# Kernel tuning notes

Hardware: AMD Instinct MI355X
Metric: run time of the kernel (lower is better)

The kernel has to match this reference:

```python
import jax, jax.numpy as jnp
import numpy as np

N = 50000   # num_entities
E = 600000  # num_edges
D = 128     # dim
R = 200     # num_relations
T = 1000    # num_timestamps
L = 2       # num_layers


def setup_inputs() -> dict:
    key = jax.random.key(0)
    ks = jax.random.split(key, 16)
    edge_index = jax.random.randint(ks[0], (2, E), 0, N)
    edge_type = jax.random.randint(ks[1], (E,), 0, R)
    edge_time = jax.random.randint(ks[2], (E,), 0, T)
    edge_weight = jax.random.uniform(ks[3], (E,), dtype=jnp.float32)
    perm = jax.random.permutation(ks[4], N)
    entity_emb = jax.random.normal(ks[5], (N, D), dtype=jnp.float32)
    rel_emb = jax.random.normal(ks[6], (R, D), dtype=jnp.float32)
    time_emb = jax.random.normal(ks[7], (T, D), dtype=jnp.float32)
    s = 1.0 / np.sqrt(D)
    in_proj_w = jax.random.uniform(ks[8], (L, D, 2 * D), minval=-s, maxval=s)
    in_proj_b = jax.random.uniform(ks[9], (L, 2 * D), minval=-s, maxval=s)
    out_proj_w = jax.random.uniform(ks[10], (L, D, D), minval=-s, maxval=s)
    out_proj_b = jax.random.uniform(ks[11], (L, D), minval=-s, maxval=s)
    A = jax.random.normal(ks[12], (L, D)) * 0.1
    B = jax.random.normal(ks[13], (L, D)) * 0.1
    ln_g = jnp.ones((L, D), dtype=jnp.float32)
    ln_b = jnp.zeros((L, D), dtype=jnp.float32)
    return dict(edge_index=edge_index, edge_type=edge_type, edge_time=edge_time,
                edge_weight=edge_weight, perm=perm, entity_emb=entity_emb,
                rel_emb=rel_emb, time_emb=time_emb, in_proj_w=in_proj_w,
                in_proj_b=in_proj_b, out_proj_w=out_proj_w, out_proj_b=out_proj_b,
                A=A, B=B, ln_g=ln_g, ln_b=ln_b)


def _mamba_layer(x, Wi, bi, Wo, bo, A, B, g_ln, b_ln):
    # x: [N, D]
    zg = x @ Wi + bi                      # [N, 2D]
    z, g = jnp.split(zg, 2, axis=-1)
    g = jax.nn.sigmoid(g)

    def step(prev, zg_i):
        z_i, g_i = zg_i
        curr = g_i * (A * prev) + B * z_i
        return curr, curr

    _, h = jax.lax.scan(step, jnp.zeros((D,), x.dtype), (z, g))  # [N, D]
    y = x + h @ Wo + bo
    mu = jnp.mean(y, axis=-1, keepdims=True)
    var = jnp.mean((y - mu) ** 2, axis=-1, keepdims=True)
    return (y - mu) / jnp.sqrt(var + 1e-5) * g_ln + b_ln


def reference(edge_index, edge_type, edge_time, edge_weight, perm, entity_emb,
              rel_emb, time_emb, in_proj_w, in_proj_b, out_proj_w, out_proj_b,
              A, B, ln_g, ln_b):
    src, dst = edge_index[0], edge_index[1]
    msgs = entity_emb[src] + rel_emb[edge_type] + time_emb[edge_time]  # [E, D]
    sums = jax.ops.segment_sum(msgs * edge_weight[:, None], dst, num_segments=N)
    cnt = jax.ops.segment_sum(edge_weight, dst, num_segments=N)
    x = sums / jnp.maximum(cnt, 1.0)[:, None]          # scatter_mean
    x = x / jnp.maximum(jnp.linalg.norm(x, axis=1, keepdims=True), 1e-12)
    x = x[perm]
    for l in range(L):
        x = _mamba_layer(x, in_proj_w[l], in_proj_b[l], out_proj_w[l],
                         out_proj_b[l], A[l], B[l], ln_g[l], ln_b[l])
    return x
```

## Files before the change

### kernel.cpp

```cpp
#include <hip/hip_runtime.h>
#include <hip/hip_bf16.h>

typedef unsigned short ushort_t;
typedef unsigned int   uint_t;
typedef __attribute__((ext_vector_type(8))) short bf8;
typedef __attribute__((ext_vector_type(4))) float f32x4;

constexpr int N = 50000;
constexpr int E = 600000;
constexpr int D = 128;
constexpr int L = 2;
constexpr int NB = (N + 255) / 256;

constexpr int RB   = 80;
constexpr int RBLK = N / RB;
constexpr int LOOK = 16;
constexpr int CSTR = 136;
constexpr int CROWS = RB + LOOK;

__device__ __forceinline__ float us2f(ushort_t u) {
    union { uint_t i; float f; } c; c.i = (uint_t)u << 16; return c.f;
}
__device__ __forceinline__ float u2f(uint_t u) {
    union { uint_t i; float f; } c; c.i = u; return c.f;
}
__device__ __forceinline__ ushort_t f2us(float f) {
    __hip_bfloat16 b = __float2bfloat16(f);
    return *(ushort_t*)&b;
}

__global__ __launch_bounds__(256) void k_alloc(
    const int* __restrict__ hist, int* __restrict__ gcnt,
    int* __restrict__ cursor, int* __restrict__ rowst)
{
    int i = blockIdx.x * 256 + threadIdx.x;
    int v = (i < N) ? hist[i] : 0;
    int lane = threadIdx.x & 63;
    int s = v;
    #pragma unroll
    for (int m = 1; m < 64; m <<= 1) {
        int t = __shfl_up(s, m, 64);
        if (lane >= m) s += t;
    }
    int base = 0;
    if (lane == 63) base = atomicAdd(gcnt, s);
    base = __shfl(base, 63, 64);
    int b = base + s - v;
    if (i < N) {
        cursor[i] = b;
        rowst[i]  = b;
    }
}

__global__ __launch_bounds__(256) void k_scatter(
    const int* __restrict__ eidx, const int* __restrict__ etype,
    const int* __restrict__ etime, const float* __restrict__ ew,
    int* __restrict__ cursor, int2* __restrict__ esort)
{
    int e = blockIdx.x * 256 + threadIdx.x;
    if (e >= E) return;
    int dst = eidx[E + e];
    int slot = atomicAdd(&cursor[dst], 1);
    int2 p;
    p.x = (eidx[e] & 0xffff) | (etype[e] << 16);
    p.y = (etime[e] & 0xffff) | ((int)f2us(ew[e]) << 16);
    esort[slot] = p;
}

constexpr size_t CAST_TBL = 3276800;
constexpr size_t CAST_W   = CAST_TBL + (size_t)L * 256 * 128
                                     + (size_t)L * 128 * 128;
constexpr size_t CAST_H   = CAST_W + E;
constexpr size_t CAST_TOT = CAST_H + N;

__global__ __launch_bounds__(256) void k_cast(
    const float* __restrict__ ent, const float* __restrict__ rel,
    const float* __restrict__ tim, const float* __restrict__ Wi,
    const float* __restrict__ Wo, const int* __restrict__ dstp,
    const int* __restrict__ perm,
    ushort_t* __restrict__ entb, ushort_t* __restrict__ relb,
    ushort_t* __restrict__ timb, ushort_t* __restrict__ WiT,
    ushort_t* __restrict__ WoT, int* __restrict__ hist,
    int* __restrict__ invp)
{
    size_t t = (size_t)blockIdx.x * 256 + threadIdx.x;
    if (t < CAST_TBL) {
        const float2* s; uint_t* d; size_t off;
        if (t < 3200000)      { s = (const float2*)ent; d = (uint_t*)entb; off = t; }
        else if (t < 3212800) { s = (const float2*)rel; d = (uint_t*)relb; off = t - 3200000; }
        else                  { s = (const float2*)tim; d = (uint_t*)timb; off = t - 3212800; }
        float2 v = s[off];
        d[off] = (uint_t)f2us(v.x) | ((uint_t)f2us(v.y) << 16);
    } else if (t < CAST_W) {
        size_t u = t - CAST_TBL;
        if (u < (size_t)L * 256 * 128) {
            int l = u / (256 * 128), r = u % (256 * 128);
            int n = r / 128, k = r % 128;
            WiT[u] = f2us(Wi[(size_t)l * 128 * 256 + k * 256 + n]);
        } else {
            size_t v = u - (size_t)L * 256 * 128;
            int l = v / (128 * 128), r = v % (128 * 128);
            int n = r / 128, k = r % 128;
            WoT[v] = f2us(Wo[(size_t)l * 128 * 128 + k * 128 + n]);
        }
    } else if (t < CAST_H) {
        int e = (int)(t - CAST_W);
        atomicAdd(&hist[dstp[e]], 1);
    } else if (t < CAST_TOT) {
        int i = (int)(t - CAST_H);
        invp[perm[i]] = i;
    }
}

__global__ __launch_bounds__(256) void k_agg(
    const int2* __restrict__ esort, const int* __restrict__ rowst,
    const int* __restrict__ hist, const int* __restrict__ invp,
    const ushort_t* __restrict__ entb, const ushort_t* __restrict__ relb,
    const ushort_t* __restrict__ timb, ushort_t* __restrict__ xbf)
{
    int wv = threadIdx.x >> 6, lane = threadIdx.x & 63;
    int d = blockIdx.x * 4 + wv;
    if (d >= N) return;
    int beg = __builtin_amdgcn_readfirstlane(rowst[d]);
    int n   = __builtin_amdgcn_readfirstlane(hist[d]);

    const uint_t* entu = (const uint_t*)entb;
    const uint_t* relu = (const uint_t*)relb;
    const uint_t* timu = (const uint_t*)timb;

    float s0[4] = {0.f, 0.f, 0.f, 0.f};
    float s1[4] = {0.f, 0.f, 0.f, 0.f};
    float wacc = 0.f;

    for (int c0 = 0; c0 < n; c0 += 64) {
        int mm = n - c0; if (mm > 64) mm = 64;
        int2 rec = esort[beg + c0 + lane];
        uint_t recx = (uint_t)rec.x, recy = (uint_t)rec.y;
        wacc += (lane < mm) ? u2f(recy & 0xffff0000u) : 0.f;

        int j = 0;
        for (; j + 3 < mm; j += 4) {
            #pragma unroll
            for (int u = 0; u < 4; u++) {
                uint_t rx = (uint_t)__builtin_amdgcn_readlane((int)recx, j + u);
                uint_t ry = (uint_t)__builtin_amdgcn_readlane((int)recy, j + u);
                const uint_t* pe = entu + ((size_t)(rx & 0xffffu) << 6);
                const uint_t* pr = relu + ((size_t)(rx >> 16) << 6);
                const uint_t* pt = timu + ((size_t)(ry & 0xffffu) << 6);
                float w = u2f(ry & 0xffff0000u);
                uint_t va = pe[lane];
                uint_t vb = pr[lane];
                uint_t vc = pt[lane];
                float lo = (u2f(va << 16) + u2f(vb << 16)) + u2f(vc << 16);
                float hi = (u2f(va & 0xffff0000u) + u2f(vb & 0xffff0000u))
                         + u2f(vc & 0xffff0000u);
                s0[u] = fmaf(lo, w, s0[u]);
                s1[u] = fmaf(hi, w, s1[u]);
            }
        }
        for (; j < mm; j++) {
            uint_t rx = (uint_t)__builtin_amdgcn_readlane((int)recx, j);
            uint_t ry = (uint_t)__builtin_amdgcn_readlane((int)recy, j);
            const uint_t* pe = entu + ((size_t)(rx & 0xffffu) << 6);
            const uint_t* pr = relu + ((size_t)(rx >> 16) << 6);
            const uint_t* pt = timu + ((size_t)(ry & 0xffffu) << 6);
            float w = u2f(ry & 0xffff0000u);
            uint_t va = pe[lane];
            uint_t vb = pr[lane];
            uint_t vc = pt[lane];
            float lo = (u2f(va << 16) + u2f(vb << 16)) + u2f(vc << 16);
            float hi = (u2f(va & 0xffff0000u) + u2f(vb & 0xffff0000u))
                     + u2f(vc & 0xffff0000u);
            s0[0] = fmaf(lo, w, s0[0]);
            s1[0] = fmaf(hi, w, s1[0]);
        }
    }
    float a0 = (s0[0] + s0[1]) + (s0[2] + s0[3]);
    float a1 = (s1[0] + s1[1]) + (s1[2] + s1[3]);

    float wsum = wacc;
    #pragma unroll
    for (int m = 32; m >= 1; m >>= 1) wsum += __shfl_xor(wsum, m, 64);

    float inv = 1.0f / fmaxf(wsum, 1.0f);
    a0 *= inv; a1 *= inv;

    float ss = a0 * a0 + a1 * a1;
    #pragma unroll
    for (int m = 32; m >= 1; m >>= 1) ss += __shfl_xor(ss, m, 64);
    float sc = 1.0f / fmaxf(sqrtf(ss), 1e-12f);

    int orow = invp[d];
    uint_t out = (uint_t)f2us(a0 * sc) | ((uint_t)f2us(a1 * sc) << 16);
    *(uint_t*)(xbf + (size_t)orow * D + 2 * lane) = out;
}

template <bool FINAL>
__global__ __launch_bounds__(256, 3) void k_layer(
    const ushort_t* __restrict__ xin, const ushort_t* __restrict__ WiT,
    const float* __restrict__ bi, const ushort_t* __restrict__ WoT,
    const float* __restrict__ bo, const float* __restrict__ Aw,
    const float* __restrict__ Bw, const float* __restrict__ lg,
    const float* __restrict__ lb, ushort_t* __restrict__ xoutb,
    float* __restrict__ outf)
{
    __shared__ ushort_t SCA[CROWS * CSTR];
    __shared__ ushort_t SCB[CROWS * CSTR];
    __shared__ float redS[16 * 4], redQ[16 * 4], muA[16], rsA[16];

    int tid = threadIdx.x;
    int w = tid >> 6, lane = tid & 63;
    int quad = lane >> 4, m = lane & 15;
    int r0 = blockIdx.x * RB;

    int cz0 = w * 32 + m, cz1 = cz0 + 16;

    float Ad0 = Aw[cz0], Bd0 = Bw[cz0];
    float Ad1 = Aw[cz1], Bd1 = Bw[cz1];
    float bz0 = bi[cz0], bz1 = bi[cz1];
    float bg0 = bi[cz0 + 128], bg1 = bi[cz1 + 128];

    const f32x4 zero4 = {0.f, 0.f, 0.f, 0.f};

    bf8 Bz0[4], Bz1[4], Bg0[4], Bg1[4];
    #pragma unroll
    for (int kb = 0; kb < 4; kb++) {
        int ko = kb * 32 + quad * 8;
        Bz0[kb] = *(const bf8*)(WiT + (size_t)cz0 * 128 + ko);
        Bz1[kb] = *(const bf8*)(WiT + (size_t)cz1 * 128 + ko);
        Bg0[kb] = *(const bf8*)(WiT + (size_t)(cz0 + 128) * 128 + ko);
        Bg1[kb] = *(const bf8*)(WiT + (size_t)(cz1 + 128) * 128 + ko);
    }

    #pragma unroll
    for (int rt = 0; rt < CROWS / 16; rt++) {
        int gr = r0 - LOOK + rt * 16 + m;
        int grc = gr < 0 ? 0 : gr;
        bf8 a[4];
        #pragma unroll
        for (int kb = 0; kb < 4; kb++)
            a[kb] = *(const bf8*)(xin + (size_t)grc * 128 + kb * 32 + quad * 8);
        f32x4 az0 = zero4, az1 = zero4, ag0 = zero4, ag1 = zero4;
        #pragma unroll
        for (int kb = 0; kb < 4; kb++) {
            az0 = __builtin_amdgcn_mfma_f32_16x16x32_bf16(a[kb], Bz0[kb], az0, 0, 0, 0);
            az1 = __builtin_amdgcn_mfma_f32_16x16x32_bf16(a[kb], Bz1[kb], az1, 0, 0, 0);
            ag0 = __builtin_amdgcn_mfma_f32_16x16x32_bf16(a[kb], Bg0[kb], ag0, 0, 0, 0);
            ag1 = __builtin_amdgcn_mfma_f32_16x16x32_bf16(a[kb], Bg1[kb], ag1, 0, 0, 0);
        }
        #pragma unroll
        for (int reg = 0; reg < 4; reg++) {
            int lr = rt * 16 + quad * 4 + reg;
            float z0 = az0[reg] + bz0, z1 = az1[reg] + bz1;
            float g0 = 1.f / (1.f + __expf(-(ag0[reg] + bg0)));
            float g1 = 1.f / (1.f + __expf(-(ag1[reg] + bg1)));
            SCA[lr * CSTR + cz0] = f2us(g0 * Ad0);
            SCB[lr * CSTR + cz0] = f2us(Bd0 * z0);
            SCA[lr * CSTR + cz1] = f2us(g1 * Ad1);
            SCB[lr * CSTR + cz1] = f2us(Bd1 * z1);
        }
    }
    __syncthreads();

    int dmm = tid & 127;
    float lca[LOOK], lcb[LOOK];
    if (tid >= 128) {
        #pragma unroll
        for (int i = 0; i < LOOK; i++) {
            lca[i] = us2f(SCA[(40 + i) * CSTR + dmm]);
            lcb[i] = us2f(SCB[(40 + i) * CSTR + dmm]);
        }
    }
    __syncthreads();

    if (tid < 128) {
        float h = 0.f;
        #pragma unroll
        for (int i = 0; i < LOOK; i++) {
            int row = r0 - LOOK + i;
            float ca = us2f(SCA[i * CSTR + tid]);
            float cb = us2f(SCB[i * CSTR + tid]);
            h = (row >= 0) ? fmaf(ca, h, cb) : 0.f;
        }
        #pragma unroll 8
        for (int i = LOOK; i < LOOK + 40; i++) {
            float ca = us2f(SCA[i * CSTR + tid]);
            float cb = us2f(SCB[i * CSTR + tid]);
            h = fmaf(ca, h, cb);
            SCA[i * CSTR + tid] = f2us(h);
        }
    } else {
        float h = 0.f;
        #pragma unroll
        for (int i = 0; i < LOOK; i++)
            h = fmaf(lca[i], h, lcb[i]);
        #pragma unroll 8
        for (int i = 56; i < 96; i++) {
            float ca = us2f(SCA[i * CSTR + dmm]);
            float cb = us2f(SCB[i * CSTR + dmm]);
            h = fmaf(ca, h, cb);
            SCA[i * CSTR + dmm] = f2us(h);
        }
    }
    __syncthreads();

    bf8 b0[4], b1[4];
    #pragma unroll
    for (int kb = 0; kb < 4; kb++) {
        int ko = kb * 32 + quad * 8;
        b0[kb] = *(const bf8*)(WoT + (size_t)cz0 * 128 + ko);
        b1[kb] = *(const bf8*)(WoT + (size_t)cz1 * 128 + ko);
    }
    float bias0 = bo[cz0], bias1 = bo[cz1];
    float gl0 = lg[cz0], gl1 = lg[cz1], bl0 = lb[cz0], bl1 = lb[cz1];

    for (int rt = 0; rt < RB / 16; rt++) {
        bf8 a[4];
        #pragma unroll
        for (int kb = 0; kb < 4; kb++)
            a[kb] = *(const bf8*)(SCA + (LOOK + rt * 16 + m) * CSTR
                                      + kb * 32 + quad * 8);
        f32x4 acc0 = {0.f, 0.f, 0.f, 0.f}, acc1 = acc0;
        #pragma unroll
        for (int kb = 0; kb < 4; kb++) {
            acc0 = __builtin_amdgcn_mfma_f32_16x16x32_bf16(a[kb], b0[kb], acc0, 0, 0, 0);
            acc1 = __builtin_amdgcn_mfma_f32_16x16x32_bf16(a[kb], b1[kb], acc1, 0, 0, 0);
        }
        float y0[4], y1[4];
        #pragma unroll
        for (int reg = 0; reg < 4; reg++) {
            int gr = r0 + rt * 16 + quad * 4 + reg;
            y0[reg] = acc0[reg] + bias0 + us2f(xin[(size_t)gr * 128 + cz0]);
            y1[reg] = acc1[reg] + bias1 + us2f(xin[(size_t)gr * 128 + cz1]);
        }
        #pragma unroll
        for (int reg = 0; reg < 4; reg++) {
            float v0 = y0[reg], v1 = y1[reg];
            float s = v0 + v1, q = v0 * v0 + v1 * v1;
            #pragma unroll
            for (int mk = 1; mk <= 8; mk <<= 1) {
                s += __shfl_xor(s, mk, 64);
                q += __shfl_xor(q, mk, 64);
            }
            if (m == 0) {
                int row = quad * 4 + reg;
                redS[row * 4 + w] = s;
                redQ[row * 4 + w] = q;
            }
        }
        __syncthreads();
        if (tid < 16) {
            float s = redS[tid * 4] + redS[tid * 4 + 1] + redS[tid * 4 + 2] + redS[tid * 4 + 3];
            float q = redQ[tid * 4] + redQ[tid * 4 + 1] + redQ[tid * 4 + 2] + redQ[tid * 4 + 3];
            float mu = s * (1.f / 128.f);
            float var = q * (1.f / 128.f) - mu * mu;
            muA[tid] = mu;
            rsA[tid] = rsqrtf(var + 1e-5f);
        }
        __syncthreads();
        #pragma unroll
        for (int reg = 0; reg < 4; reg++) {
            int rr = quad * 4 + reg;
            int gr = r0 + rt * 16 + rr;
            float mu = muA[rr], rs = rsA[rr];
            float v0 = (y0[reg] - mu) * rs * gl0 + bl0;
            float v1 = (y1[reg] - mu) * rs * gl1 + bl1;
            if (FINAL) {
                outf[(size_t)gr * 128 + cz0] = v0;
                outf[(size_t)gr * 128 + cz1] = v1;
            } else {
                xoutb[(size_t)gr * 128 + cz0] = f2us(v0);
                xoutb[(size_t)gr * 128 + cz1] = f2us(v1);
            }
        }
    }
}

extern "C" void kernel_launch(void* const* d_in, const int* in_sizes, int n_in,
                              void* d_out, int out_size, void* d_ws, size_t ws_size,
                              hipStream_t stream)
{
    const int*   eidx  = (const int*)d_in[0];
    const int*   etype = (const int*)d_in[1];
    const int*   etime = (const int*)d_in[2];
    const float* ew    = (const float*)d_in[3];
    const int*   perm  = (const int*)d_in[4];
    const float* ent   = (const float*)d_in[5];
    const float* rel   = (const float*)d_in[6];
    const float* tim   = (const float*)d_in[7];
    const float* Wi    = (const float*)d_in[8];
    const float* bi    = (const float*)d_in[9];
    const float* Wo    = (const float*)d_in[10];
    const float* bo    = (const float*)d_in[11];
    const float* Aw    = (const float*)d_in[12];
    const float* Bw    = (const float*)d_in[13];
    const float* lg    = (const float*)d_in[14];
    const float* lbp   = (const float*)d_in[15];

    char* base = (char*)d_ws;
    size_t o = 0;
    ushort_t* xbf  = (ushort_t*)(base + o); o += (size_t)N * D * 2;
    ushort_t* xb2  = (ushort_t*)(base + o); o += (size_t)N * D * 2;
    ushort_t* entb = (ushort_t*)(base + o); o += (size_t)N * D * 2;
    ushort_t* relb = (ushort_t*)(base + o); o += (size_t)200 * D * 2;
    ushort_t* timb = (ushort_t*)(base + o); o += (size_t)1000 * D * 2;
    ushort_t* WiT  = (ushort_t*)(base + o); o += (size_t)L * 256 * 128 * 2;
    ushort_t* WoT  = (ushort_t*)(base + o); o += (size_t)L * 128 * 128 * 2;
    int2*     esort  = (int2*)(base + o);   o += (size_t)E * 8;
    int*      hist   = (int*)(base + o);    o += (size_t)N * 4;
    int*      gcnt   = (int*)(base + o);    o += 4;
    int*      cursor = (int*)(base + o);    o += (size_t)N * 4;
    int*      rowst  = (int*)(base + o);    o += (size_t)N * 4;
    int*      invp   = (int*)(base + o);    o += (size_t)N * 4;

    hipMemsetAsync(hist, 0, (N + 1) * sizeof(int), stream);

    k_cast    <<<(int)((CAST_TOT + 255) / 256), 256, 0, stream>>>(
                  ent, rel, tim, Wi, Wo, eidx + E, perm,
                  entb, relb, timb, WiT, WoT, hist, invp);
    k_alloc   <<<NB, 256, 0, stream>>>(hist, gcnt, cursor, rowst);
    k_scatter <<<(E + 255) / 256, 256, 0, stream>>>(eidx, etype, etime, ew,
                                                    cursor, esort);
    k_agg     <<<(N + 3) / 4, 256, 0, stream>>>(esort, rowst, hist, invp,
                                                entb, relb, timb, xbf);

    k_layer<false><<<RBLK, 256, 0, stream>>>(
        xbf, WiT, bi, WoT, bo, Aw, Bw, lg, lbp, xb2, nullptr);
    k_layer<true><<<RBLK, 256, 0, stream>>>(
        xb2, WiT + (size_t)256 * 128, bi + 256, WoT + (size_t)128 * 128,
        bo + 128, Aw + 128, Bw + 128, lg + 128, lbp + 128,
        nullptr, (float*)d_out);
}
```

Measured before the change: 283.5 us.

## Fuse preprocessing and layer kernels into persistent kernels with grid barriers

Merges the cast, histogram prefix-alloc, scatter and aggregation kernels into one persistent kernel of 512 blocks separated by software grid barriers. The two layer kernels become one persistent kernel of 416 blocks that loops over row tiles and places a grid barrier between the layers. The aim is to cut kernel launch gaps and tail effects. In exchange it adds barrier spin overhead, reduces occupancy control, and relies on every block being co-resident for the barriers to avoid deadlock.

Result: slower. 845.1 us (+198.1%).

```diff
diff --git a/kernel.cpp b/kernel.cpp
--- a/kernel.cpp
+++ b/kernel.cpp
@@ -10,7 +10,6 @@
 constexpr int E = 600000;
 constexpr int D = 128;
 constexpr int L = 2;
-constexpr int NB = (N + 255) / 256;
 
 constexpr int RB   = 80;
 constexpr int RBLK = N / RB;
@@ -18,54 +17,10 @@
 constexpr int CSTR = 136;
 constexpr int CROWS = RB + LOOK;
 
-__device__ __forceinline__ float us2f(ushort_t u) {
-    union { uint_t i; float f; } c; c.i = (uint_t)u << 16; return c.f;
-}
-__device__ __forceinline__ float u2f(uint_t u) {
-    union { uint_t i; float f; } c; c.i = u; return c.f;
-}
-__device__ __forceinline__ ushort_t f2us(float f) {
-    __hip_bfloat16 b = __float2bfloat16(f);
-    return *(ushort_t*)&b;
-}
-
-__global__ __launch_bounds__(256) void k_alloc(
-    const int* __restrict__ hist, int* __restrict__ gcnt,
-    int* __restrict__ cursor, int* __restrict__ rowst)
-{
-    int i = blockIdx.x * 256 + threadIdx.x;
-    int v = (i < N) ? hist[i] : 0;
-    int lane = threadIdx.x & 63;
-    int s = v;
-    #pragma unroll
-    for (int m = 1; m < 64; m <<= 1) {
-        int t = __shfl_up(s, m, 64);
-        if (lane >= m) s += t;
-    }
-    int base = 0;
-    if (lane == 63) base = atomicAdd(gcnt, s);
-    base = __shfl(base, 63, 64);
-    int b = base + s - v;
-    if (i < N) {
-        cursor[i] = b;
-        rowst[i]  = b;
-    }
-}
-
-__global__ __launch_bounds__(256) void k_scatter(
-    const int* __restrict__ eidx, const int* __restrict__ etype,
-    const int* __restrict__ etime, const float* __restrict__ ew,
-    int* __restrict__ cursor, int2* __restrict__ esort)
-{
-    int e = blockIdx.x * 256 + threadIdx.x;
-    if (e >= E) return;
-    int dst = eidx[E + e];
-    int slot = atomicAdd(&cursor[dst], 1);
-    int2 p;
-    p.x = (eidx[e] & 0xffff) | (etype[e] << 16);
-    p.y = (etime[e] & 0xffff) | ((int)f2us(ew[e]) << 16);
-    esort[slot] = p;
-}
+constexpr int PREB = 512;
+constexpr int PRET = PREB * 256;
+constexpr int PREW = PREB * 4;
+constexpr int LBLK = 416;
 
 constexpr size_t CAST_TBL = 3276800;
 constexpr size_t CAST_W   = CAST_TBL + (size_t)L * 256 * 128
@@ -73,130 +28,199 @@
 constexpr size_t CAST_H   = CAST_W + E;
 constexpr size_t CAST_TOT = CAST_H + N;
 
-__global__ __launch_bounds__(256) void k_cast(
-    const float* __restrict__ ent, const float* __restrict__ rel,
-    const float* __restrict__ tim, const float* __restrict__ Wi,
-    const float* __restrict__ Wo, const int* __restrict__ dstp,
-    const int* __restrict__ perm,
+__device__ __forceinline__ float us2f(ushort_t u) {
+    union { uint_t i; float f; } c; c.i = (uint_t)u << 16; return c.f;
+}
+__device__ __forceinline__ float u2f(uint_t u) {
+    union { uint_t i; float f; } c; c.i = u; return c.f;
+}
+__device__ __forceinline__ ushort_t f2us(float f) {
+    __hip_bfloat16 b = __float2bfloat16(f);
+    return *(ushort_t*)&b;
+}
+
+__device__ __forceinline__ void gridbar(int* bar, int nb) {
+    __threadfence();
+    __syncthreads();
+    if (threadIdx.x == 0) {
+        int g = __hip_atomic_load(&bar[1], __ATOMIC_ACQUIRE,
+                                  __HIP_MEMORY_SCOPE_AGENT);
+        if (atomicAdd(&bar[0], 1) == nb - 1) {
+            __hip_atomic_store(&bar[0], 0, __ATOMIC_RELAXED,
+                               __HIP_MEMORY_SCOPE_AGENT);
+            __hip_atomic_store(&bar[1], g + 1, __ATOMIC_RELEASE,
+                               __HIP_MEMORY_SCOPE_AGENT);
+        } else {
+            while (__hip_atomic_load(&bar[1], __ATOMIC_ACQUIRE,
+                                     __HIP_MEMORY_SCOPE_AGENT) == g)
+                __builtin_amdgcn_s_sleep(2);
+        }
+    }
+    __syncthreads();
+    __threadfence();
+}
+
+__global__ __launch_bounds__(256, 4) void k_pre(
+    const int* __restrict__ eidx, const int* __restrict__ etype,
+    const int* __restrict__ etime, const float* __restrict__ ew,
+    const int* __restrict__ perm, const float* __restrict__ ent,
+    const float* __restrict__ rel, const float* __restrict__ tim,
+    const float* __restrict__ Wi, const float* __restrict__ Wo,
     ushort_t* __restrict__ entb, ushort_t* __restrict__ relb,
     ushort_t* __restrict__ timb, ushort_t* __restrict__ WiT,
     ushort_t* __restrict__ WoT, int* __restrict__ hist,
-    int* __restrict__ invp)
+    int* __restrict__ gcnt, int* __restrict__ bar,
+    int* __restrict__ cursor, int* __restrict__ rowst,
+    int* __restrict__ invp, int2* __restrict__ esort,
+    ushort_t* __restrict__ xbf)
 {
-    size_t t = (size_t)blockIdx.x * 256 + threadIdx.x;
-    if (t < CAST_TBL) {
-        const float2* s; uint_t* d; size_t off;
-        if (t < 3200000)      { s = (const float2*)ent; d = (uint_t*)entb; off = t; }
-        else if (t < 3212800) { s = (const float2*)rel; d = (uint_t*)relb; off = t - 3200000; }
-        else                  { s = (const float2*)tim; d = (uint_t*)timb; off = t - 3212800; }
-        float2 v = s[off];
-        d[off] = (uint_t)f2us(v.x) | ((uint_t)f2us(v.y) << 16);
-    } else if (t < CAST_W) {
-        size_t u = t - CAST_TBL;
-        if (u < (size_t)L * 256 * 128) {
-            int l = u / (256 * 128), r = u % (256 * 128);
-            int n = r / 128, k = r % 128;
-            WiT[u] = f2us(Wi[(size_t)l * 128 * 256 + k * 256 + n]);
+    int tid  = threadIdx.x;
+    int gidx = blockIdx.x * 256 + tid;
+    int lane = tid & 63;
+    int gw   = blockIdx.x * 4 + (tid >> 6);
+    const int* dstp = eidx + E;
+
+    for (size_t t = gidx; t < CAST_TOT; t += PRET) {
+        if (t < CAST_TBL) {
+            const float2* s; uint_t* d; size_t off;
+            if (t < 3200000)      { s = (const float2*)ent; d = (uint_t*)entb; off = t; }
+            else if (t < 3212800) { s = (const float2*)rel; d = (uint_t*)relb; off = t - 3200000; }
+            else                  { s = (const float2*)tim; d = (uint_t*)timb; off = t - 3212800; }
+            float2 v = s[off];
+            d[off] = (uint_t)f2us(v.x) | ((uint_t)f2us(v.y) << 16);
+        } else if (t < CAST_W) {
+            size_t u = t - CAST_TBL;
+            if (u < (size_t)L * 256 * 128) {
+                int l = u / (256 * 128), r = u % (256 * 128);
+                int n = r / 128, k = r % 128;
+                WiT[u] = f2us(Wi[(size_t)l * 128 * 256 + k * 256 + n]);
+            } else {
+                size_t v = u - (size_t)L * 256 * 128;
+                int l = v / (128 * 128), r = v % (128 * 128);
+                int n = r / 128, k = r % 128;
+                WoT[v] = f2us(Wo[(size_t)l * 128 * 128 + k * 128 + n]);
+            }
+        } else if (t < CAST_H) {
+            int e = (int)(t - CAST_W);
+            atomicAdd(&hist[dstp[e]], 1);
         } else {
-            size_t v = u - (size_t)L * 256 * 128;
-            int l = v / (128 * 128), r = v % (128 * 128);
-            int n = r / 128, k = r % 128;
-            WoT[v] = f2us(Wo[(size_t)l * 128 * 128 + k * 128 + n]);
-        }
-    } else if (t < CAST_H) {
-        int e = (int)(t - CAST_W);
-        atomicAdd(&hist[dstp[e]], 1);
-    } else if (t < CAST_TOT) {
-        int i = (int)(t - CAST_H);
-        invp[perm[i]] = i;
-    }
-}
-
-__global__ __launch_bounds__(256) void k_agg(
-    const int2* __restrict__ esort, const int* __restrict__ rowst,
-    const int* __restrict__ hist, const int* __restrict__ invp,
-    const ushort_t* __restrict__ entb, const ushort_t* __restrict__ relb,
-    const ushort_t* __restrict__ timb, ushort_t* __restrict__ xbf)
-{
-    int wv = threadIdx.x >> 6, lane = threadIdx.x & 63;
-    int d = blockIdx.x * 4 + wv;
-    if (d >= N) return;
-    int beg = __builtin_amdgcn_readfirstlane(rowst[d]);
-    int n   = __builtin_amdgcn_readfirstlane(hist[d]);
-
-    const uint_t* entu = (const uint_t*)entb;
-    const uint_t* relu = (const uint_t*)relb;
-    const uint_t* timu = (const uint_t*)timb;
-
-    float s0[4] = {0.f, 0.f, 0.f, 0.f};
-    float s1[4] = {0.f, 0.f, 0.f, 0.f};
-    float wacc = 0.f;
-
-    for (int c0 = 0; c0 < n; c0 += 64) {
-        int mm = n - c0; if (mm > 64) mm = 64;
-        int2 rec = esort[beg + c0 + lane];
-        uint_t recx = (uint_t)rec.x, recy = (uint_t)rec.y;
-        wacc += (lane < mm) ? u2f(recy & 0xffff0000u) : 0.f;
-
-        int j = 0;
-        for (; j + 3 < mm; j += 4) {
+            int i = (int)(t - CAST_H);
+            invp[perm[i]] = i;
+        }
+    }
+    gridbar(bar, PREB);
+
+    for (int c = gw; c * 64 < N; c += PREW) {
+        int i = c * 64 + lane;
+        int v = (i < N) ? hist[i] : 0;
+        int s = v;
+        #pragma unroll
+        for (int m = 1; m < 64; m <<= 1) {
+            int t = __shfl_up(s, m, 64);
+            if (lane >= m) s += t;
+        }
+        int base = 0;
+        if (lane == 63) base = atomicAdd(gcnt, s);
+        base = __shfl(base, 63, 64);
+        int b = base + s - v;
+        if (i < N) {
+            cursor[i] = b;
+            rowst[i]  = b;
+        }
+    }
+    gridbar(bar, PREB);
+
+    for (int e = gidx; e < E; e += PRET) {
+        int dst = dstp[e];
+        int slot = atomicAdd(&cursor[dst], 1);
+        int2 p;
+        p.x = (eidx[e] & 0xffff) | (etype[e] << 16);
+        p.y = (etime[e] & 0xffff) | ((int)f2us(ew[e]) << 16);
+        esort[slot] = p;
+    }
+    gridbar(bar, PREB);
+
+    {
+        const uint_t* entu = (const uint_t*)entb;
+        const uint_t* relu = (const uint_t*)relb;
+        const uint_t* timu = (const uint_t*)timb;
+        for (int d = gw; d < N; d += PREW) {
+            int beg = __builtin_amdgcn_readfirstlane(rowst[d]);
+            int n   = __builtin_amdgcn_readfirstlane(hist[d]);
+
+            float s0[4] = {0.f, 0.f, 0.f, 0.f};
+            float s1[4] = {0.f, 0.f, 0.f, 0.f};
+            float wacc = 0.f;
+
+            for (int c0 = 0; c0 < n; c0 += 64) {
+                int mm = n - c0; if (mm > 64) mm = 64;
+                int2 rec = esort[beg + c0 + lane];
+                uint_t recx = (uint_t)rec.x, recy = (uint_t)rec.y;
+                wacc += (lane < mm) ? u2f(recy & 0xffff0000u) : 0.f;
+
+                int j = 0;
+                for (; j + 3 < mm; j += 4) {
+                    #pragma unroll
+                    for (int u = 0; u < 4; u++) {
+                        uint_t rx = (uint_t)__builtin_amdgcn_readlane((int)recx, j + u);
+                        uint_t ry = (uint_t)__builtin_amdgcn_readlane((int)recy, j + u);
+                        const uint_t* pe = entu + ((size_t)(rx & 0xffffu) << 6);
+                        const uint_t* pr = relu + ((size_t)(rx >> 16) << 6);
+                        const uint_t* pt = timu + ((size_t)(ry & 0xffffu) << 6);
+                        float w = u2f(ry & 0xffff0000u);
+                        uint_t va = pe[lane];
+                        uint_t vb = pr[lane];
+                        uint_t vc = pt[lane];
+                        float lo = (u2f(va << 16) + u2f(vb << 16)) + u2f(vc << 16);
+                        float hi = (u2f(va & 0xffff0000u) + u2f(vb & 0xffff0000u))
+                                 + u2f(vc & 0xffff0000u);
+                        s0[u] = fmaf(lo, w, s0[u]);
+                        s1[u] = fmaf(hi, w, s1[u]);
+                    }
+                }
+                for (; j < mm; j++) {
+                    uint_t rx = (uint_t)__builtin_amdgcn_readlane((int)recx, j);
+                    uint_t ry = (uint_t)__builtin_amdgcn_readlane((int)recy, j);
+                    const uint_t* pe = entu + ((size_t)(rx & 0xffffu) << 6);
+                    const uint_t* pr = relu + ((size_t)(rx >> 16) << 6);
+                    const uint_t* pt = timu + ((size_t)(ry & 0xffffu) << 6);
+                    float w = u2f(ry & 0xffff0000u);
+                    uint_t va = pe[lane];
+                    uint_t vb = pr[lane];
+                    uint_t vc = pt[lane];
+                    float lo = (u2f(va << 16) + u2f(vb << 16)) + u2f(vc << 16);
+                    float hi = (u2f(va & 0xffff0000u) + u2f(vb & 0xffff0000u))
+                             + u2f(vc & 0xffff0000u);
+                    s0[0] = fmaf(lo, w, s0[0]);
+                    s1[0] = fmaf(hi, w, s1[0]);
+                }
+            }
+            float a0 = (s0[0] + s0[1]) + (s0[2] + s0[3]);
+            float a1 = (s1[0] + s1[1]) + (s1[2] + s1[3]);
+
+            float wsum = wacc;
             #pragma unroll
-            for (int u = 0; u < 4; u++) {
-                uint_t rx = (uint_t)__builtin_amdgcn_readlane((int)recx, j + u);
-                uint_t ry = (uint_t)__builtin_amdgcn_readlane((int)recy, j + u);
-                const uint_t* pe = entu + ((size_t)(rx & 0xffffu) << 6);
-                const uint_t* pr = relu + ((size_t)(rx >> 16) << 6);
-                const uint_t* pt = timu + ((size_t)(ry & 0xffffu) << 6);
-                float w = u2f(ry & 0xffff0000u);
-                uint_t va = pe[lane];
-                uint_t vb = pr[lane];
-                uint_t vc = pt[lane];
-                float lo = (u2f(va << 16) + u2f(vb << 16)) + u2f(vc << 16);
-                float hi = (u2f(va & 0xffff0000u) + u2f(vb & 0xffff0000u))
-                         + u2f(vc & 0xffff0000u);
-                s0[u] = fmaf(lo, w, s0[u]);
-                s1[u] = fmaf(hi, w, s1[u]);
-            }
-        }
-        for (; j < mm; j++) {
-            uint_t rx = (uint_t)__builtin_amdgcn_readlane((int)recx, j);
-            uint_t ry = (uint_t)__builtin_amdgcn_readlane((int)recy, j);
-            const uint_t* pe = entu + ((size_t)(rx & 0xffffu) << 6);
-            const uint_t* pr = relu + ((size_t)(rx >> 16) << 6);
-            const uint_t* pt = timu + ((size_t)(ry & 0xffffu) << 6);
-            float w = u2f(ry & 0xffff0000u);
-            uint_t va = pe[lane];
-            uint_t vb = pr[lane];
-            uint_t vc = pt[lane];
-            float lo = (u2f(va << 16) + u2f(vb << 16)) + u2f(vc << 16);
-            float hi = (u2f(va & 0xffff0000u) + u2f(vb & 0xffff0000u))
-                     + u2f(vc & 0xffff0000u);
-            s0[0] = fmaf(lo, w, s0[0]);
-            s1[0] = fmaf(hi, w, s1[0]);
-        }
-    }
-    float a0 = (s0[0] + s0[1]) + (s0[2] + s0[3]);
-    float a1 = (s1[0] + s1[1]) + (s1[2] + s1[3]);
-
-    float wsum = wacc;
-    #pragma unroll
-    for (int m = 32; m >= 1; m >>= 1) wsum += __shfl_xor(wsum, m, 64);
-
-    float inv = 1.0f / fmaxf(wsum, 1.0f);
-    a0 *= inv; a1 *= inv;
-
-    float ss = a0 * a0 + a1 * a1;
-    #pragma unroll
-    for (int m = 32; m >= 1; m >>= 1) ss += __shfl_xor(ss, m, 64);
-    float sc = 1.0f / fmaxf(sqrtf(ss), 1e-12f);
-
-    int orow = invp[d];
-    uint_t out = (uint_t)f2us(a0 * sc) | ((uint_t)f2us(a1 * sc) << 16);
-    *(uint_t*)(xbf + (size_t)orow * D + 2 * lane) = out;
+            for (int m = 32; m >= 1; m >>= 1) wsum += __shfl_xor(wsum, m, 64);
+
+            float inv = 1.0f / fmaxf(wsum, 1.0f);
+            a0 *= inv; a1 *= inv;
+
+            float ss = a0 * a0 + a1 * a1;
+            #pragma unroll
+            for (int m = 32; m >= 1; m >>= 1) ss += __shfl_xor(ss, m, 64);
+            float sc = 1.0f / fmaxf(sqrtf(ss), 1e-12f);
+
+            int orow = invp[d];
+            uint_t out = (uint_t)f2us(a0 * sc) | ((uint_t)f2us(a1 * sc) << 16);
+            *(uint_t*)(xbf + (size_t)orow * D + 2 * lane) = out;
+        }
+    }
 }
 
 template <bool FINAL>
-__global__ __launch_bounds__(256, 3) void k_layer(
+__device__ __forceinline__ void layer_body(
+    int r0, ushort_t* SCA, ushort_t* SCB, float* redS, float* redQ,
+    float* muA, float* rsA,
     const ushort_t* __restrict__ xin, const ushort_t* __restrict__ WiT,
     const float* __restrict__ bi, const ushort_t* __restrict__ WoT,
     const float* __restrict__ bo, const float* __restrict__ Aw,
@@ -204,14 +228,9 @@
     const float* __restrict__ lb, ushort_t* __restrict__ xoutb,
     float* __restrict__ outf)
 {
-    __shared__ ushort_t SCA[CROWS * CSTR];
-    __shared__ ushort_t SCB[CROWS * CSTR];
-    __shared__ float redS[16 * 4], redQ[16 * 4], muA[16], rsA[16];
-
     int tid = threadIdx.x;
     int w = tid >> 6, lane = tid & 63;
     int quad = lane >> 4, m = lane & 15;
-    int r0 = blockIdx.x * RB;
 
     int cz0 = w * 32 + m, cz1 = cz0 + 16;
 
@@ -373,6 +392,35 @@
                 xoutb[(size_t)gr * 128 + cz1] = f2us(v1);
             }
         }
+    }
+}
+
+__global__ __launch_bounds__(256, 2) void k_layers(
+    const ushort_t* __restrict__ xbf, ushort_t* __restrict__ xb2,
+    const ushort_t* __restrict__ WiT, const float* __restrict__ bi,
+    const ushort_t* __restrict__ WoT, const float* __restrict__ bo,
+    const float* __restrict__ Aw, const float* __restrict__ Bw,
+    const float* __restrict__ lg, const float* __restrict__ lb,
+    int* __restrict__ bar, float* __restrict__ outf)
+{
+    __shared__ ushort_t SCA[CROWS * CSTR];
+    __shared__ ushort_t SCB[CROWS * CSTR];
+    __shared__ float redS[16 * 4], redQ[16 * 4], muA[16], rsA[16];
+
+    for (int t = blockIdx.x; t < RBLK; t += LBLK) {
+        __syncthreads();
+        layer_body<false>(t * RB, SCA, SCB, redS, redQ, muA, rsA,
+                          xbf, WiT, bi, WoT, bo, Aw, Bw, lg, lb,
+                          xb2, nullptr);
+    }
+    gridbar(bar, LBLK);
+    for (int t = blockIdx.x; t < RBLK; t += LBLK) {
+        __syncthreads();
+        layer_body<true>(t * RB, SCA, SCB, redS, redQ, muA, rsA,
+                         xb2, WiT + (size_t)256 * 128, bi + 256,
+                         WoT + (size_t)128 * 128, bo + 128,
+                         Aw + 128, Bw + 128, lg + 128, lb + 128,
+                         nullptr, outf);
     }
 }
 
@@ -409,25 +457,19 @@
     int2*     esort  = (int2*)(base + o);   o += (size_t)E * 8;
     int*      hist   = (int*)(base + o);    o += (size_t)N * 4;
     int*      gcnt   = (int*)(base + o);    o += 4;
+    int*      barA   = (int*)(base + o);    o += 8;
+    int*      barB   = (int*)(base + o);    o += 8;
     int*      cursor = (int*)(base + o);    o += (size_t)N * 4;
     int*      rowst  = (int*)(base + o);    o += (size_t)N * 4;
     int*      invp   = (int*)(base + o);    o += (size_t)N * 4;
 
-    hipMemsetAsync(hist, 0, (N + 1) * sizeof(int), stream);
-
-    k_cast    <<<(int)((CAST_TOT + 255) / 256), 256, 0, stream>>>(
-                  ent, rel, tim, Wi, Wo, eidx + E, perm,
-                  entb, relb, timb, WiT, WoT, hist, invp);
-    k_alloc   <<<NB, 256, 0, stream>>>(hist, gcnt, cursor, rowst);
-    k_scatter <<<(E + 255) / 256, 256, 0, stream>>>(eidx, etype, etime, ew,
-                                                    cursor, esort);
-    k_agg     <<<(N + 3) / 4, 256, 0, stream>>>(esort, rowst, hist, invp,
-                                                entb, relb, timb, xbf);
-
-    k_layer<false><<<RBLK, 256, 0, stream>>>(
-        xbf, WiT, bi, WoT, bo, Aw, Bw, lg, lbp, xb2, nullptr);
-    k_layer<true><<<RBLK, 256, 0, stream>>>(
-        xb2, WiT + (size_t)256 * 128, bi + 256, WoT + (size_t)128 * 128,
-        bo + 128, Aw + 128, Bw + 128, lg + 128, lbp + 128,
-        nullptr, (float*)d_out);
-}
+    hipMemsetAsync(hist, 0, (N + 5) * sizeof(int), stream);
+
+    k_pre<<<PREB, 256, 0, stream>>>(
+        eidx, etype, etime, ew, perm, ent, rel, tim, Wi, Wo,
+        entb, relb, timb, WiT, WoT, hist, gcnt, barA,
+        cursor, rowst, invp, esort, xbf);
+
+    k_layers<<<LBLK, 256, 0, stream>>>(
+        xbf, xb2, WiT, bi, WoT, bo, Aw, Bw, lg, lbp, barB, (float*)d_out);
+}
```
